# Optimization experiments

Measured on AMD Instinct MI355X. Metric: run time of the kernel, lower is better.

The kernel has to match this reference:

```python
import jax, jax.numpy as jnp
import numpy as np

POOL_SIZE = 512
TOPK = 8
PRE_SEQ_LEN = 32
HIDDEN = 1024
EPS = 1e-8  # torch cosine_similarity eps


def setup_inputs() -> dict:
    key = jax.random.key(0)
    k1, k2, k3 = jax.random.split(key, 3)
    querys = jax.random.normal(k1, (1024, HIDDEN), dtype=jnp.float32)
    # learned params: keys initialized zeros in torch, but use randn so cosine is non-degenerate
    prompts_key = jax.random.normal(k2, (POOL_SIZE, HIDDEN), dtype=jnp.float32)
    prompts = jax.random.uniform(k3, (POOL_SIZE, PRE_SEQ_LEN, HIDDEN), dtype=jnp.float32)
    return {"querys": querys, "prompts_key": prompts_key, "prompts": prompts}


def reference(querys, prompts_key, prompts):
    # cosine similarity: [B, P]
    qn = querys / jnp.maximum(jnp.linalg.norm(querys, axis=-1, keepdims=True), EPS)
    kn = prompts_key / jnp.maximum(jnp.linalg.norm(prompts_key, axis=-1, keepdims=True), EPS)
    similarity = jnp.einsum('bh,ph->bp', qn, kn)
    # topk (sorted descending, like torch.topk); gathered sims equal topk values
    top_sim, indices = jax.lax.top_k(similarity, TOPK)  # [B, K], [B, K]
    gathered_prompts = jnp.take(prompts, indices, axis=0)  # [B, K, L, H]
    return gathered_prompts, top_sim
```

## Files before the change

kernel.cpp:

```cpp
#include <hip/hip_runtime.h>
#include <math.h>

#define NB 1024
#define NP 512
#define NH 1024
#define NK 8
#define NL 32
#define NBK (NB * NK)
#define SLICE (NL * NH)
#define EPSF 1e-8f

typedef float f32x4 __attribute__((ext_vector_type(4)));
typedef short s16x8 __attribute__((ext_vector_type(8)));
typedef unsigned short u16;

__device__ __forceinline__ u16 f2bf(float x) {
  union { float f; unsigned u; } v; v.f = x;
  unsigned r = (v.u + 0x7FFFu + ((v.u >> 16) & 1u)) >> 16;
  return (u16)r;
}
__device__ __forceinline__ float bf2f(u16 b) {
  union { unsigned u; float f; } v; v.u = ((unsigned)b) << 16;
  return v.f;
}

__global__ __launch_bounds__(256) void convert_kernel(
    const float* __restrict__ q, const float* __restrict__ pk,
    u16* __restrict__ Q3, u16* __restrict__ K3) {
  const int row = blockIdx.x;
  const int tid = threadIdx.x;
  const float* src;
  u16* dst;
  int plane;
  if (row < NB) {
    src = q + (size_t)row * NH;
    dst = Q3 + (size_t)row * NH;
    plane = NB * NH;
  } else {
    src = pk + (size_t)(row - NB) * NH;
    dst = K3 + (size_t)(row - NB) * NH;
    plane = NP * NH;
  }
  float4 v = ((const float4*)src)[tid];
  float s = v.x * v.x + v.y * v.y + v.z * v.z + v.w * v.w;
#pragma unroll
  for (int off = 32; off; off >>= 1) s += __shfl_xor(s, off);
  __shared__ float ws[4];
  if ((tid & 63) == 0) ws[tid >> 6] = s;
  __syncthreads();
  float total = ws[0] + ws[1] + ws[2] + ws[3];
  const float inv = 1.f / fmaxf(sqrtf(total), EPSF);

  float x[4] = {v.x * inv, v.y * inv, v.z * inv, v.w * inv};
  u16 t0[4], t1[4], t2[4];
#pragma unroll
  for (int i = 0; i < 4; ++i) {
    float f = x[i];
    u16 b0 = f2bf(f);        float r1 = f - bf2f(b0);
    u16 b1 = f2bf(r1);       float r2 = r1 - bf2f(b1);
    u16 b2 = f2bf(r2);
    t0[i] = b0; t1[i] = b1; t2[i] = b2;
  }
  ushort4* d0 = (ushort4*)(dst + tid * 4);
  ushort4* d1 = (ushort4*)(dst + plane + tid * 4);
  ushort4* d2 = (ushort4*)(dst + 2 * plane + tid * 4);
  *d0 = make_ushort4(t0[0], t0[1], t0[2], t0[3]);
  *d1 = make_ushort4(t1[0], t1[1], t1[2], t1[3]);
  *d2 = make_ushort4(t2[0], t2[1], t2[2], t2[3]);
}

__global__ __launch_bounds__(256) void sim_mfma_kernel(
    const u16* __restrict__ Q3, const u16* __restrict__ K3,
    float* __restrict__ sim) {
  const int bm = blockIdx.x;
  const int bn = blockIdx.y;
  const int wave = threadIdx.x >> 6;
  const int lane = threadIdx.x & 63;
  const int r0 = bm * 32 + (wave & 1) * 16;
  const int c0 = bn * 32 + (wave >> 1) * 16;
  const int koff = (lane >> 4) * 8;

  const u16* aB = Q3 + (size_t)(r0 + (lane & 15)) * NH + koff;
  const u16* bB = K3 + (size_t)(c0 + (lane & 15)) * NH + koff;
  const int QP = NB * NH, KP = NP * NH;

  f32x4 acc0 = {0.f, 0.f, 0.f, 0.f};
  f32x4 acc1 = {0.f, 0.f, 0.f, 0.f};

  for (int kc = 0; kc < NH; kc += 64) {
    s16x8 a00 = *(const s16x8*)(aB + kc);
    s16x8 a01 = *(const s16x8*)(aB + QP + kc);
    s16x8 a02 = *(const s16x8*)(aB + 2 * QP + kc);
    s16x8 b00 = *(const s16x8*)(bB + kc);
    s16x8 b01 = *(const s16x8*)(bB + KP + kc);
    s16x8 b02 = *(const s16x8*)(bB + 2 * KP + kc);
    s16x8 a10 = *(const s16x8*)(aB + kc + 32);
    s16x8 a11 = *(const s16x8*)(aB + QP + kc + 32);
    s16x8 a12 = *(const s16x8*)(aB + 2 * QP + kc + 32);
    s16x8 b10 = *(const s16x8*)(bB + kc + 32);
    s16x8 b11 = *(const s16x8*)(bB + KP + kc + 32);
    s16x8 b12 = *(const s16x8*)(bB + 2 * KP + kc + 32);

    acc0 = __builtin_amdgcn_mfma_f32_16x16x32_bf16(a00, b00, acc0, 0, 0, 0);
    acc1 = __builtin_amdgcn_mfma_f32_16x16x32_bf16(a10, b10, acc1, 0, 0, 0);
    acc0 = __builtin_amdgcn_mfma_f32_16x16x32_bf16(a00, b01, acc0, 0, 0, 0);
    acc1 = __builtin_amdgcn_mfma_f32_16x16x32_bf16(a10, b11, acc1, 0, 0, 0);
    acc0 = __builtin_amdgcn_mfma_f32_16x16x32_bf16(a01, b00, acc0, 0, 0, 0);
    acc1 = __builtin_amdgcn_mfma_f32_16x16x32_bf16(a11, b10, acc1, 0, 0, 0);
    acc0 = __builtin_amdgcn_mfma_f32_16x16x32_bf16(a01, b01, acc0, 0, 0, 0);
    acc1 = __builtin_amdgcn_mfma_f32_16x16x32_bf16(a11, b11, acc1, 0, 0, 0);
    acc0 = __builtin_amdgcn_mfma_f32_16x16x32_bf16(a00, b02, acc0, 0, 0, 0);
    acc1 = __builtin_amdgcn_mfma_f32_16x16x32_bf16(a10, b12, acc1, 0, 0, 0);
    acc0 = __builtin_amdgcn_mfma_f32_16x16x32_bf16(a02, b00, acc0, 0, 0, 0);
    acc1 = __builtin_amdgcn_mfma_f32_16x16x32_bf16(a12, b10, acc1, 0, 0, 0);
  }

#pragma unroll
  for (int i = 0; i < 4; ++i) {
    int row = r0 + (lane >> 4) * 4 + i;
    int col = c0 + (lane & 15);
    sim[(size_t)row * NP + col] = acc0[i] + acc1[i];
  }
}

__global__ __launch_bounds__(256) void topk_kernel(
    const float* __restrict__ sim, float* __restrict__ top_sim, int* __restrict__ top_idx) {
  int row = blockIdx.x * 4 + (threadIdx.x >> 6);
  int lane = threadIdx.x & 63;
  if (row >= NB) return;

  float vals[NP / 64];
#pragma unroll
  for (int i = 0; i < NP / 64; ++i) vals[i] = sim[(size_t)row * NP + lane + i * 64];

  for (int t = 0; t < NK; ++t) {
    float bv = vals[0];
    int bi = 0;
#pragma unroll
    for (int i = 1; i < NP / 64; ++i) {
      if (vals[i] > bv) { bv = vals[i]; bi = i; }
    }
    float v = bv;
    int p = lane + bi * 64;
#pragma unroll
    for (int off = 32; off; off >>= 1) {
      float ov = __shfl_xor(v, off);
      int op = __shfl_xor(p, off);
      if (ov > v || (ov == v && op < p)) { v = ov; p = op; }
    }
    if (lane == 0) {
      top_sim[row * NK + t] = v;
      top_idx[row * NK + t] = p;
    }
    if ((p & 63) == lane) {
      int wi = p >> 6;
#pragma unroll
      for (int i = 0; i < NP / 64; ++i)
        if (i == wi) vals[i] = -INFINITY;
    }
  }
}

__global__ __launch_bounds__(512) void sortperm_kernel(
    const int* __restrict__ idx, int* __restrict__ order) {
  __shared__ int hist[NP];
  __shared__ int offs[NP];
  const int t = threadIdx.x;
  hist[t] = 0;
  __syncthreads();
  for (int i = t; i < NBK; i += 512) atomicAdd(&hist[idx[i]], 1);
  __syncthreads();
  int sum = 0;
  for (int i = 0; i < t; ++i) sum += hist[i];
  offs[t] = sum;
  __syncthreads();
  for (int i = t; i < NBK; i += 512) {
    int p = idx[i];
    int pos = atomicAdd(&offs[p], 1);
    order[pos] = (i << 16) | p;
  }
}

__global__ __launch_bounds__(256) void gather_sorted(
    const float* __restrict__ prompts, const int* __restrict__ order,
    float* __restrict__ out, int skip_slice) {
  const int d = blockIdx.x;
  const int s = (d & 7) * (NBK / 8) + (d >> 3);
  const int packed = order[s];
  const int j = packed >> 16;
  if (j == skip_slice) return;
  const int p = packed & 0xFFFF;
  const f32x4* __restrict__ src = (const f32x4*)(prompts + (size_t)p * SLICE);
  f32x4* __restrict__ dst = (f32x4*)(out + (size_t)j * SLICE);
  const int t = threadIdx.x;
#pragma unroll
  for (int i = 0; i < (SLICE / 4) / 256; ++i) {
    f32x4 v = src[t + i * 256];
    __builtin_nontemporal_store(v, &dst[t + i * 256]);
  }
}

__global__ __launch_bounds__(256) void gather_tail(
    const float* __restrict__ prompts, const int* __restrict__ idx,
    float* __restrict__ out, int j) {
  const int p = idx[j];
  __syncthreads();
  const f32x4* __restrict__ src = (const f32x4*)(prompts + (size_t)p * SLICE);
  f32x4* __restrict__ dst = (f32x4*)(out + (size_t)j * SLICE);
  const int t = threadIdx.x;
#pragma unroll
  for (int i = 0; i < (SLICE / 4) / 256; ++i) {
    f32x4 v = src[t + i * 256];
    __builtin_nontemporal_store(v, &dst[t + i * 256]);
  }
}

extern "C" void kernel_launch(void* const* d_in, const int* in_sizes, int n_in,
                              void* d_out, int out_size, void* d_ws, size_t ws_size,
                              hipStream_t stream) {
  const float* querys = (const float*)d_in[0];
  const float* prompts_key = (const float*)d_in[1];
  const float* prompts = (const float*)d_in[2];
  float* out = (float*)d_out;

  const size_t GATHER = (size_t)NBK * SLICE;
  float* top_sim = out + GATHER;

  float* sim = out;
  u16* Q3 = (u16*)(out + 524288);
  u16* K3 = (u16*)(out + 2097152);

  int* idx;
  int* order;
  int skip_slice;
  if (ws_size >= 2 * NBK * sizeof(int)) {
    idx = (int*)d_ws;
    order = idx + NBK;
    skip_slice = -1;
  } else {
    idx = (int*)(out + (size_t)(NBK - 2) * SLICE);
    order = idx + NBK;
    skip_slice = NBK - 2;
  }

  convert_kernel<<<NB + NP, 256, 0, stream>>>(querys, prompts_key, Q3, K3);

  dim3 gsim(NB / 32, NP / 32);
  sim_mfma_kernel<<<gsim, 256, 0, stream>>>(Q3, K3, sim);

  topk_kernel<<<NB / 4, 256, 0, stream>>>(sim, top_sim, idx);

  sortperm_kernel<<<1, 512, 0, stream>>>(idx, order);

  gather_sorted<<<NBK, 256, 0, stream>>>(prompts, order, out, skip_slice);

  if (skip_slice >= 0) {
    gather_tail<<<1, 256, 0, stream>>>(prompts, idx, out, skip_slice);
  }
}
```

Baseline: 292.9 us.

## Broadcast gathered prompt chunks across groups of sorted outputs to reuse loads

Replaces the one-block-per-output-slice gather with blocks that each handle one chunk of a slice for a group of eight consecutive sorted entries. When consecutive entries share the same prompt index, the chunk is kept in registers and stored to every destination without being reloaded. The intent is to cut redundant reads of the prompts tensor. The catch is that each block now does eight serial store rounds and uses more registers.

```diff
diff --git a/kernel.cpp b/kernel.cpp
--- a/kernel.cpp
+++ b/kernel.cpp
@@ -9,6 +9,9 @@
 #define NBK (NB * NK)
 #define SLICE (NL * NH)
 #define EPSF 1e-8f
+#define GG 8
+#define CH 8
+#define CHUNK (SLICE / CH)
 
 typedef float f32x4 __attribute__((ext_vector_type(4)));
 typedef short s16x8 __attribute__((ext_vector_type(8)));
@@ -181,22 +184,36 @@
   }
 }
 
-__global__ __launch_bounds__(256) void gather_sorted(
+__global__ __launch_bounds__(256) void gather_bcast(
     const float* __restrict__ prompts, const int* __restrict__ order,
     float* __restrict__ out, int skip_slice) {
   const int d = blockIdx.x;
-  const int s = (d & 7) * (NBK / 8) + (d >> 3);
-  const int packed = order[s];
-  const int j = packed >> 16;
-  if (j == skip_slice) return;
-  const int p = packed & 0xFFFF;
-  const f32x4* __restrict__ src = (const f32x4*)(prompts + (size_t)p * SLICE);
-  f32x4* __restrict__ dst = (f32x4*)(out + (size_t)j * SLICE);
+  const int xcd = d & 7;
+  const int i = d >> 3;
+  const int gl = i >> 3;
+  const int c = i & 7;
+  const int g = xcd * (NBK / GG / 8) + gl;
   const int t = threadIdx.x;
-#pragma unroll
-  for (int i = 0; i < (SLICE / 4) / 256; ++i) {
-    f32x4 v = src[t + i * 256];
-    __builtin_nontemporal_store(v, &dst[t + i * 256]);
+  const int base = c * CHUNK + t * 4;
+
+  f32x4 r0, r1, r2, r3;
+  int pprev = -1;
+#pragma unroll
+  for (int k = 0; k < GG; ++k) {
+    const int packed = order[g * GG + k];
+    const int j = packed >> 16;
+    const int p = packed & 0xFFFF;
+    if (p != pprev) {
+      const f32x4* src = (const f32x4*)(prompts + (size_t)p * SLICE + base);
+      r0 = src[0]; r1 = src[256]; r2 = src[512]; r3 = src[768];
+      pprev = p;
+    }
+    if (j == skip_slice) continue;
+    f32x4* dst = (f32x4*)(out + (size_t)j * SLICE + base);
+    __builtin_nontemporal_store(r0, &dst[0]);
+    __builtin_nontemporal_store(r1, &dst[256]);
+    __builtin_nontemporal_store(r2, &dst[512]);
+    __builtin_nontemporal_store(r3, &dst[768]);
   }
 }
 
@@ -252,7 +269,7 @@
 
   sortperm_kernel<<<1, 512, 0, stream>>>(idx, order);
 
-  gather_sorted<<<NBK, 256, 0, stream>>>(prompts, order, out, skip_slice);
+  gather_bcast<<<(NBK / GG) * CH, 256, 0, stream>>>(prompts, order, out, skip_slice);
 
   if (skip_slice >= 0) {
     gather_tail<<<1, 256, 0, stream>>>(prompts, idx, out, skip_slice);
```

After: 276.9 us. -5.4%, faster.
